# Kernel optimization log

Measured on AMD Instinct MI355X. Metric: run time of the kernel, lower is better.

Reference implementation:

```python
import jax, jax.numpy as jnp
import numpy as np
from jax import lax

NC = 80          # len(model.names)
MAX_DET = 300    # args.max_det
TOPK = 1500      # max_det * 5 candidate prune (static-shape stand-in for conf mask)
CONF = 0.25      # args.conf
IOU_TH = 0.45    # args.iou
IMGSZ = 640.0    # max(x.shape[2:])
B, A = 32, 8400  # batch, anchors for 640x640 YOLOv8


def setup_inputs() -> dict:
    key = jax.random.key(0)
    kb, kw, ks = jax.random.split(key, 3)
    # realistic xyxy boxes inside a 640x640 image
    x1y1 = jax.random.uniform(kb, (B, A, 2), dtype=jnp.float32) * 600.0
    wh = 5.0 + jax.random.uniform(kw, (B, A, 2), dtype=jnp.float32) * 35.0
    boxes = jnp.concatenate([x1y1, x1y1 + wh], axis=-1)          # [B, A, 4]
    cls_scores = jax.random.uniform(ks, (B, A, NC), dtype=jnp.float32)
    pred = jnp.concatenate([boxes, cls_scores], axis=-1)          # [B, A, 4+NC]
    return {"pred": pred.transpose(0, 2, 1)}                      # [B, 4+NC, A]


def box_iou(a, b):
    # a: [K,4] xyxy, b: [K,4] xyxy -> [K,K]
    lt = jnp.maximum(a[:, None, :2], b[None, :, :2])
    rb = jnp.minimum(a[:, None, 2:], b[None, :, 2:])
    inter = jnp.prod(jnp.clip(rb - lt, 0.0), axis=-1)
    area_a = jnp.prod(a[:, 2:] - a[:, :2], axis=-1)
    area_b = jnp.prod(b[:, 2:] - b[:, :2], axis=-1)
    return inter / (area_a[:, None] + area_b[None, :] - inter + 1e-7)


def _nms_image(boxes, scores, classes):
    # boxes [A,4], scores [A], classes [A] (int)
    valid = scores > CONF                       # score > args.conf mask
    msc = jnp.where(valid, scores, -1.0)
    _, idx = lax.top_k(msc, TOPK)               # score-desc candidate prune
    box = boxes[idx]
    cls = classes[idx]
    score = scores[idx]
    valid = valid[idx]
    # normalize + per-class offset trick (agnostic_nms=False, end=4, multiplier=1/nc)
    mult = 1.0 / NC
    nmsbox = box * (mult / IMGSZ)
    nmsbox = nmsbox + (cls.astype(box.dtype) * mult)[:, None]
    iou = box_iou(nmsbox, nmsbox)               # [TOPK, TOPK]
    ar = jnp.arange(TOPK)

    def step(i, supp):
        # greedy NMS: box i survives if not suppressed by an earlier kept box
        keep_i = jnp.logical_not(supp[i]) & valid[i]
        return supp | (keep_i & (iou[i] > IOU_TH) & (ar > i))

    supp = lax.fori_loop(0, TOPK, step, jnp.zeros((TOPK,), dtype=bool))
    keep = jnp.logical_not(supp) & valid
    # stable sort: kept boxes first (already score-ordered), take max_det, zero-pad rest
    order = jnp.argsort(jnp.where(keep, 0, 1).astype(jnp.int32))
    sel = order[:MAX_DET]
    m = keep[sel].astype(box.dtype)[:, None]
    dets = jnp.concatenate(
        [box[sel], score[sel][:, None], cls[sel].astype(box.dtype)[:, None]], axis=-1
    )                                            # [MAX_DET, 6]
    return dets * m


def reference(pred):
    # pred: [B, 4+NC, A]
    p = pred.transpose(0, 2, 1)                  # [B, A, 4+NC]
    boxes = p[..., :4]
    cls_scores = p[..., 4:4 + NC]
    scores = cls_scores.max(axis=-1)             # scores, classes = scores.max(dim=-1)
    classes = jnp.argmax(cls_scores, axis=-1)
    return jax.vmap(_nms_image)(boxes, scores, classes)  # [B, MAX_DET, 6]
```

## Files before the change

kernel.cpp:

```cpp
#include <hip/hip_runtime.h>
#include <stdint.h>

typedef unsigned long long u64;
typedef unsigned int u32;

#define NCLS 80
#define NA   8400
#define NIMG 32
#define TOPK 1500
#define MAXDET 300
#define NW 24
#define NBLK 24
#define ROWPAD (NBLK * 64)
#define CONF 0.25f
#define IOU_TH 0.45f

#define CHUNK 2048
#define NCH   5
#define CAND  1500

#define OFF_CAND   ((size_t)0)
#define OFF_TBOX   (OFF_CAND + (size_t)NIMG*NCH*CAND*8)
#define OFF_TNMS   (OFF_TBOX + (size_t)NIMG*TOPK*16)
#define OFF_TSC    (OFF_TNMS + (size_t)NIMG*TOPK*16)
#define OFF_TCL    (OFF_TSC  + (size_t)NIMG*TOPK*4)
#define OFF_MASK   (OFF_TCL  + (size_t)NIMG*TOPK*4)
#define WS_NEED    (OFF_MASK + (size_t)NIMG*ROWPAD*NW*8)


__global__ __launch_bounds__(1024) void k_sortchunk(const float* __restrict__ pred,
                                                    u64* __restrict__ cand) {
    __shared__ u64 s[CHUNK];
    const int tid = threadIdx.x;
    const int c = blockIdx.x;
    const int b = blockIdx.y;
    const int a0 = c * CHUNK;
    const float* pb = pred + (size_t)b * (4 + NCLS) * NA;

    for (int i = tid; i < CHUNK; i += 1024) {
        int a = a0 + i;
        u64 key = ~0ULL;
        if (a < NA) {
            float best = pb[(size_t)4 * NA + a];
            int bi = 0;
#pragma unroll 8
            for (int cc = 1; cc < NCLS; ++cc) {
                float v = pb[(size_t)(4 + cc) * NA + a];
                if (v > best) { best = v; bi = cc; }
            }
            float msc = (best > CONF) ? best : -1.0f;
            u32 u = __float_as_uint(msc);
            u = (u & 0x80000000u) ? ~u : (u | 0x80000000u);
            key = ((u64)(~u) << 32) | ((u64)(u32)a << 18) | ((u64)(u32)bi << 11);
        }
        s[i] = key;
    }
    __syncthreads();

    for (u32 k = 2; k <= CHUNK; k <<= 1) {
        for (u32 j = k >> 1; j > 0; j >>= 1) {
            int t = tid;
            int i = 2 * t - (t & (j - 1));
            u64 x = s[i], y = s[i + j];
            bool asc = (i & k) == 0;
            if ((x > y) == asc) { s[i] = y; s[i + j] = x; }
            __syncthreads();
        }
    }

    u64* cb = cand + ((size_t)b * NCH + c) * CAND;
    for (int i = tid; i < CAND; i += 1024) cb[i] = s[i];
}

__global__ __launch_bounds__(1024) void k_merge_gather(const float* __restrict__ pred,
                                                       const u64* __restrict__ cand,
                                                       float4* __restrict__ tbox,
                                                       float4* __restrict__ tnms,
                                                       float* __restrict__ tsc,
                                                       int* __restrict__ tcl) {
#pragma clang fp contract(off)
    __shared__ u64 sA[CHUNK];
    __shared__ u64 sB[CHUNK];
    const int tid = threadIdx.x;
    const int b = blockIdx.x;
    const u64* cb = cand + (size_t)b * NCH * CAND;

    for (int i = tid; i < CHUNK; i += 1024)
        sA[i] = (i < CAND) ? cb[i] : ~0ULL;

    for (int m = 1; m < NCH; ++m) {
        for (int i = tid; i < CHUNK; i += 1024)
            sB[i] = (i < CAND) ? cb[(size_t)m * CAND + i] : ~0ULL;
        __syncthreads();
        for (int i = tid; i < CHUNK; i += 1024) {
            u64 x = sA[i], y = sB[CHUNK - 1 - i];
            sA[i] = (x < y) ? x : y;
        }
        __syncthreads();
        for (u32 j = CHUNK >> 1; j > 0; j >>= 1) {
            int t = tid;
            int i = 2 * t - (t & (j - 1));
            u64 x = sA[i], y = sA[i + j];
            if (x > y) { sA[i] = y; sA[i + j] = x; }
            __syncthreads();
        }
    }

    const float* pb = pred + (size_t)b * (4 + NCLS) * NA;
    const float C1 = (float)((1.0 / 80.0) / 640.0);
    const float C2 = (float)(1.0 / 80.0);
    for (int r = tid; r < TOPK; r += 1024) {
        u64 key = sA[r];
        int a = (int)((key >> 18) & 0x3FFFu);
        int cl = (int)((key >> 11) & 0x7Fu);
        u32 ou = ~((u32)(key >> 32));
        u32 fb = (ou & 0x80000000u) ? (ou ^ 0x80000000u) : ~ou;
        float msc = __uint_as_float(fb);
        float x1 = pb[a], y1 = pb[NA + a], x2 = pb[2 * NA + a], y2 = pb[3 * NA + a];
        float off = (float)cl * C2;
        tbox[b * TOPK + r] = make_float4(x1, y1, x2, y2);
        tnms[b * TOPK + r] = make_float4(x1 * C1 + off, y1 * C1 + off,
                                         x2 * C1 + off, y2 * C1 + off);
        tsc[b * TOPK + r] = msc;
        tcl[b * TOPK + r] = cl;
    }
}

__global__ __launch_bounds__(256) void k_mask(const float4* __restrict__ tnms,
                                              u64* __restrict__ mask) {
#pragma clang fp contract(off)
    __shared__ float4 nb[ROWPAD];
    const int b = blockIdx.y;
    const int tid = threadIdx.x;
    for (int i = tid; i < ROWPAD; i += 256)
        nb[i] = (i < TOPK) ? tnms[b * TOPK + i]
                           : make_float4(0.0f, 0.0f, 0.0f, 0.0f);
    __syncthreads();

    const int r0 = blockIdx.x * 64;
    const int r = r0 + (tid & 63);
    const int q = tid >> 6;
    const float4 bi = nb[r];
    const float area_i = (bi.z - bi.x) * (bi.w - bi.y);

    u64* mrow = mask + ((size_t)b * ROWPAD + r) * NW;
#pragma unroll
    for (int wi = 0; wi < 6; ++wi) {
        const int w = q + wi * 4;
        u64 bits = 0ULL;
        if (w * 64 + 63 > r0) {
            const int j0 = w * 64;
#pragma unroll 8
            for (int l = 0; l < 64; ++l) {
                const int j = j0 + l;
                float4 bj = nb[j];
                float lx = fmaxf(bi.x, bj.x), ly = fmaxf(bi.y, bj.y);
                float rx = fminf(bi.z, bj.z), ry = fminf(bi.w, bj.w);
                float iw = fmaxf(rx - lx, 0.0f), ih = fmaxf(ry - ly, 0.0f);
                float inter = iw * ih;
                float area_j = (bj.z - bj.x) * (bj.w - bj.y);
                float iou = inter / (area_i + area_j - inter + 1e-7f);
                bits |= ((iou > IOU_TH) && (j > r)) ? (1ULL << l) : 0ULL;
            }
        }
        mrow[w] = bits;
    }
}

__device__ __forceinline__ void dense_block(const u64* ss, int t, u64& acc, int ml) {
    const int lane = threadIdx.x;
    u64 rword = ss[lane * NW + t];
    u64 dead = __shfl(acc, t);
    u64 kb = 0ULL;
#pragma unroll
    for (int ii = 0; ii < 64; ++ii) {
        u32 rlo = (u32)__builtin_amdgcn_readlane((int)(u32)(rword & 0xFFFFFFFFu), ii);
        u32 rhi = (u32)__builtin_amdgcn_readlane((int)(u32)(rword >> 32), ii);
        u64 row = ((u64)rhi << 32) | rlo;
        if (!((dead >> ii) & 1ULL)) { dead |= row; kb |= (1ULL << ii); }
    }
    u64 a0 = 0, a1 = 0, a2 = 0, a3 = 0;
#pragma unroll
    for (int q = 0; q < 16; ++q) {
        u64 v0 = ss[(4 * q + 0) * NW + ml];
        u64 v1 = ss[(4 * q + 1) * NW + ml];
        u64 v2 = ss[(4 * q + 2) * NW + ml];
        u64 v3 = ss[(4 * q + 3) * NW + ml];
        a0 |= ((kb >> (4 * q + 0)) & 1ULL) ? v0 : 0ULL;
        a1 |= ((kb >> (4 * q + 1)) & 1ULL) ? v1 : 0ULL;
        a2 |= ((kb >> (4 * q + 2)) & 1ULL) ? v2 : 0ULL;
        a3 |= ((kb >> (4 * q + 3)) & 1ULL) ? v3 : 0ULL;
    }
    acc |= a0 | a1 | a2 | a3;
}

__device__ __forceinline__ void step_block(uint4 (&R)[12], int t, u64& acc, int ml,
                                           const uint4* g4, u64* sbuf) {
    const int lane = threadIdx.x;
    u32 nz = 0;
#pragma unroll
    for (int i = 0; i < 12; ++i) nz |= (R[i].x | R[i].y | R[i].z | R[i].w);
    const u64 anym = __ballot(nz != 0);
    if (anym) {
        uint4* l4 = (uint4*)sbuf;
#pragma unroll
        for (int i = 0; i < 12; ++i) l4[i * 64 + lane] = R[i];
    }
    if (t + 2 < NBLK) {
#pragma unroll
        for (int i = 0; i < 12; ++i) R[i] = g4[(size_t)(t + 2) * 768 + i * 64 + lane];
    }
    if (anym) dense_block(sbuf, t, acc, ml);
}

__global__ __launch_bounds__(64) void k_scan(const u64* __restrict__ mask,
                                             const float4* __restrict__ tbox,
                                             const float* __restrict__ tsc,
                                             const int* __restrict__ tcl,
                                             float* __restrict__ out) {
    __shared__ u64 sbuf[64 * NW];
    const int b = blockIdx.x;
    const int lane = threadIdx.x;
    float* outb = out + (size_t)b * MAXDET * 6;
    for (int i = lane; i < MAXDET * 6; i += 64) outb[i] = 0.0f;
    __syncthreads();

    u64 validw = 0ULL;
    if (lane < NW) {
        const float4* t4 = (const float4*)(tsc + (size_t)b * TOPK);
#pragma unroll
        for (int q = 0; q < 16; ++q) {
            int i4 = lane * 16 + q;
            if (i4 < TOPK / 4) {
                float4 v = t4[i4];
                int base = q * 4;
                if (v.x > CONF) validw |= (1ULL << (base + 0));
                if (v.y > CONF) validw |= (1ULL << (base + 1));
                if (v.z > CONF) validw |= (1ULL << (base + 2));
                if (v.w > CONF) validw |= (1ULL << (base + 3));
            }
        }
    }
    u64 acc = (lane < NW) ? ~validw : ~0ULL;

    const u64* mbase = mask + (size_t)b * ROWPAD * NW;
    const uint4* g4 = (const uint4*)mbase;
    const int ml = (lane < NW) ? lane : 0;

    uint4 rA[12], rB[12];
#pragma unroll
    for (int i = 0; i < 12; ++i) rA[i] = g4[0 * 768 + i * 64 + lane];
#pragma unroll
    for (int i = 0; i < 12; ++i) rB[i] = g4[1 * 768 + i * 64 + lane];

    for (int tt = 0; tt < 12; ++tt) {
        step_block(rA, 2 * tt,     acc, ml, g4, sbuf);
        step_block(rB, 2 * tt + 1, acc, ml, g4, sbuf);
    }

    u64 keepw = (lane < NW) ? ~acc : 0ULL;
    int cnt = __popcll(keepw);
    int pre = cnt;
#pragma unroll
    for (int d = 1; d < 64; d <<= 1) {
        int o = __shfl_up(pre, d);
        if (lane >= d) pre += o;
    }
    int rbase = pre - cnt;
    u64 m = keepw;
    int idx = 0;
    while (m) {
        int l = __ffsll((long long)m) - 1;
        m &= m - 1;
        int r = rbase + idx; ++idx;
        if (r < MAXDET) {
            int j = lane * 64 + l;
            float4 bx = tbox[b * TOPK + j];
            float sc = tsc[b * TOPK + j];
            int c = tcl[b * TOPK + j];
            float* o6 = outb + r * 6;
            o6[0] = bx.x; o6[1] = bx.y; o6[2] = bx.z; o6[3] = bx.w;
            o6[4] = sc;   o6[5] = (float)c;
        }
    }
}

extern "C" void kernel_launch(void* const* d_in, const int* in_sizes, int n_in,
                              void* d_out, int out_size, void* d_ws, size_t ws_size,
                              hipStream_t stream) {
    const float* pred = (const float*)d_in[0];
    float* out = (float*)d_out;
    char* ws = (char*)d_ws;
    if (ws_size < WS_NEED) return;

    u64*    cand = (u64*)   (ws + OFF_CAND);
    float4* tbox = (float4*)(ws + OFF_TBOX);
    float4* tnms = (float4*)(ws + OFF_TNMS);
    float*  tsc  = (float*) (ws + OFF_TSC);
    int*    tcl  = (int*)   (ws + OFF_TCL);
    u64*    mask = (u64*)   (ws + OFF_MASK);

    k_sortchunk<<<dim3(NCH, NIMG), 1024, 0, stream>>>(pred, cand);
    k_merge_gather<<<NIMG, 1024, 0, stream>>>(pred, cand, tbox, tnms, tsc, tcl);
    k_mask<<<dim3(NBLK, NIMG), 256, 0, stream>>>(tnms, mask);
    k_scan<<<NIMG, 64, 0, stream>>>(mask, tbox, tsc, tcl, out);
}
```

Baseline: 255.2 us.

## Split IoU mask kernel into column halves and skip division on disjoint boxes

The IoU bitmask kernel now launches 36 blocks per image instead of 24. Each block loads only half of the candidate boxes (768) into shared memory and computes 3 column words instead of 6. Column halves that are entirely below the diagonal are handled by the other blocks, which write zeros for them, so the more expensive upper-triangle work is spread across more blocks. A wave-wide ballot also skips the area and division path when no lane has a positive intersection, trading an extra vote per pair for fewer divides in the many disjoint cases.

```diff
diff --git a/kernel.cpp b/kernel.cpp
--- a/kernel.cpp
+++ b/kernel.cpp
@@ -129,41 +129,53 @@
 __global__ __launch_bounds__(256) void k_mask(const float4* __restrict__ tnms,
                                               u64* __restrict__ mask) {
 #pragma clang fp contract(off)
-    __shared__ float4 nb[ROWPAD];
+    __shared__ float4 nb[768];
     const int b = blockIdx.y;
+    const int idx = blockIdx.x;
+    const int z = (idx < 24) ? 1 : 0;
+    const int rb = (idx < 24) ? idx : (idx - 24);
+    const int c0 = z * 768;
     const int tid = threadIdx.x;
-    for (int i = tid; i < ROWPAD; i += 256)
-        nb[i] = (i < TOPK) ? tnms[b * TOPK + i]
+
+    for (int i = tid; i < 768; i += 256) {
+        int j = c0 + i;
+        nb[i] = (j < TOPK) ? tnms[b * TOPK + j]
                            : make_float4(0.0f, 0.0f, 0.0f, 0.0f);
+    }
     __syncthreads();
 
-    const int r0 = blockIdx.x * 64;
+    const int r0 = rb * 64;
     const int r = r0 + (tid & 63);
     const int q = tid >> 6;
-    const float4 bi = nb[r];
+    float4 bi = (r < TOPK) ? tnms[b * TOPK + r]
+                           : make_float4(0.0f, 0.0f, 0.0f, 0.0f);
     const float area_i = (bi.z - bi.x) * (bi.w - bi.y);
 
     u64* mrow = mask + ((size_t)b * ROWPAD + r) * NW;
 #pragma unroll
-    for (int wi = 0; wi < 6; ++wi) {
-        const int w = q + wi * 4;
+    for (int wi = 0; wi < 3; ++wi) {
+        const int w = z * 12 + q + wi * 4;
         u64 bits = 0ULL;
         if (w * 64 + 63 > r0) {
+            const int jbase = (w - z * 12) * 64;
             const int j0 = w * 64;
-#pragma unroll 8
+#pragma unroll 4
             for (int l = 0; l < 64; ++l) {
-                const int j = j0 + l;
-                float4 bj = nb[j];
+                float4 bj = nb[jbase + l];
                 float lx = fmaxf(bi.x, bj.x), ly = fmaxf(bi.y, bj.y);
                 float rx = fminf(bi.z, bj.z), ry = fminf(bi.w, bj.w);
                 float iw = fmaxf(rx - lx, 0.0f), ih = fmaxf(ry - ly, 0.0f);
                 float inter = iw * ih;
-                float area_j = (bj.z - bj.x) * (bj.w - bj.y);
-                float iou = inter / (area_i + area_j - inter + 1e-7f);
-                bits |= ((iou > IOU_TH) && (j > r)) ? (1ULL << l) : 0ULL;
+                if (__ballot(inter > 0.0f)) {
+                    float area_j = (bj.z - bj.x) * (bj.w - bj.y);
+                    float iou = inter / (area_i + area_j - inter + 1e-7f);
+                    bits |= ((iou > IOU_TH) && (j0 + l > r)) ? (1ULL << l) : 0ULL;
+                }
             }
         }
         mrow[w] = bits;
+        if (z == 1 && r0 >= 768)
+            mrow[w - 12] = 0ULL;
     }
 }
 
@@ -302,6 +314,6 @@
 
     k_sortchunk<<<dim3(NCH, NIMG), 1024, 0, stream>>>(pred, cand);
     k_merge_gather<<<NIMG, 1024, 0, stream>>>(pred, cand, tbox, tnms, tsc, tcl);
-    k_mask<<<dim3(NBLK, NIMG), 256, 0, stream>>>(tnms, mask);
+    k_mask<<<dim3(36, NIMG), 256, 0, stream>>>(tnms, mask);
     k_scan<<<NIMG, 64, 0, stream>>>(mask, tbox, tsc, tcl, out);
 }
```

New measurement: 236.4 us. -7.4%, faster.
